# Optimization experiments

Measured on AMD Instinct MI355X. Metric: run time of the kernel, lower is better.

## Reference

```python
import jax, jax.numpy as jnp
import numpy as np

B, V, T, R = 128, 128000, 4096, 64
REP_PENALTY = 1.2   # _rep_penalty (set_repetition_penalty)
MAX_REPS = 3        # _max_reps
REQUIRED_BOOST = 5.0  # _required_boost


def setup_inputs() -> dict:
    key = jax.random.key(0)
    k1, k2, k3, k4 = jax.random.split(key, 4)
    logits = jax.random.normal(k1, (B, V), dtype=jnp.float32)
    generated_so_far = jax.random.randint(k2, (B, T), 0, V, dtype=jnp.int32)
    forbidden_mask = jax.random.bernoulli(k3, 0.01, (V,))
    required_tokens = jax.random.randint(k4, (R,), 0, V, dtype=jnp.int32)
    return {"logits": logits, "generated_so_far": generated_so_far,
            "forbidden_mask": forbidden_mask, "required_tokens": required_tokens}


def reference(logits, generated_so_far, forbidden_mask, required_tokens):
    Bn, Vn = logits.shape
    neg_inf = jnp.float32(-jnp.inf)

    # 1) forbidden tokens -> -inf
    out = jnp.where(forbidden_mask[None, :], neg_inf, logits)

    # per-row token occurrence counts (vectorized bincount) [B, V]
    counts = jnp.zeros((Bn, Vn), jnp.int32).at[
        jnp.arange(Bn)[:, None], generated_so_far
    ].add(1)

    # 2) boost required tokens not yet generated and not forbidden
    present = counts[:, required_tokens] > 0              # [B, R]
    allowed = ~forbidden_mask[required_tokens]            # [R]
    boost = jnp.where((~present) & allowed[None, :],
                      jnp.float32(REQUIRED_BOOST), jnp.float32(0.0))
    out = out.at[:, required_tokens].add(boost)

    # 3) repetition penalty on tokens with count >= MAX_REPS (skip -inf)
    penalized = jnp.where(out > 0, out / REP_PENALTY, out * REP_PENALTY)
    out = jnp.where((counts >= MAX_REPS) & (out != neg_inf), penalized, out)
    return out
```

## Files before the change

### kernel.cpp

```cpp
#include <hip/hip_runtime.h>
#include <cstdint>
#include <cstddef>

#define BB 128
#define VV 128000
#define TT 4096
#define SS 16
#define VR (VV / SS)
#define HW (VR / 4)
#define NT 256

typedef float vf4 __attribute__((ext_vector_type(4)));

__global__ __launch_bounds__(NT) void enforce_kernel(
    const float* __restrict__ logits,
    const int*  __restrict__ gen,
    const unsigned char* __restrict__ maskb,
    const int*  __restrict__ req,
    float* __restrict__ out,
    int R)
{
  __shared__ unsigned hist[HW];
  __shared__ unsigned reqw[HW];
  __shared__ unsigned flz;
  const int tid = threadIdx.x;

  const int L    = blockIdx.x;
  const int xcd  = L & 7;
  const int q    = L >> 3;
  const int s    = q & (SS - 1);
  const int b    = (q >> 4) * 8 + xcd;
  const int vbase = s * VR;

  const int4* grow = (const int4*)(gen + b * TT);
  const int4 g0 = grow[tid];
  const int4 g1 = grow[tid + NT];
  const int4 g2 = grow[tid + 2 * NT];
  const int4 g3 = grow[tid + 3 * NT];
  const int rt = (tid < R) ? req[tid] : -1;

  for (int i = tid; i < HW; i += NT) { hist[i] = 0u; reqw[i] = 0u; }
  if (tid < 64) {
    const uint4* md = (const uint4*)maskb;
    unsigned a = 0u, c = 0u;
#pragma unroll
    for (int k = 0; k < 16; ++k) {
      uint4 w = md[tid + k * 64];
      unsigned o = w.x | w.y | w.z | w.w;
      a |= o & 0x000000FFu;
      c |= o & 0xFFFFFF00u;
    }
    unsigned long long ba = __ballot(a != 0u);
    unsigned long long bc = __ballot(c != 0u);
    if (tid == 0) flz = (ba ? 1u : 0u) | (bc ? 2u : 0u);
  }
  __syncthreads();

  const unsigned agg = flz;
  const int ml = (agg & 2u) ? ((agg & 1u) ? 1 : 2) : ((agg & 1u) ? 0 : 1);

  bool rforb = true;
  if (rt >= 0) {
    if (ml == 1)      rforb = (maskb[rt] != 0);
    else if (ml == 0) rforb = (((const int*)maskb)[rt] != 0);
    else              rforb = (((const float*)maskb)[rt] != 0.0f);
  }

  {
    const int t4[16] = {g0.x, g0.y, g0.z, g0.w, g1.x, g1.y, g1.z, g1.w,
                        g2.x, g2.y, g2.z, g2.w, g3.x, g3.y, g3.z, g3.w};
#pragma unroll
    for (int j = 0; j < 16; ++j) {
      unsigned d = (unsigned)(t4[j] - vbase);
      if (d < (unsigned)VR)
        atomicAdd(&hist[d >> 2], 1u << ((d & 3u) * 8u));
    }
  }

  if (rt >= 0 && !rforb) {
    unsigned d = (unsigned)(rt - vbase);
    if (d < (unsigned)VR)
      atomicAdd(&reqw[d >> 2], 1u << ((d & 3u) * 8u));
  }
  for (int r = tid + NT; r < R; r += NT) {
    int t = req[r];
    unsigned d = (unsigned)(t - vbase);
    if (d < (unsigned)VR) {
      bool fb;
      if (ml == 1)      fb = (maskb[t] != 0);
      else if (ml == 0) fb = (((const int*)maskb)[t] != 0);
      else              fb = (((const float*)maskb)[t] != 0.0f);
      if (!fb) atomicAdd(&reqw[d >> 2], 1u << ((d & 3u) * 8u));
    }
  }
  __syncthreads();

  const vf4* lrow = (const vf4*)(logits + (size_t)b * VV + vbase);
  vf4*       orow = (vf4*)(out + (size_t)b * VV + vbase);
  const unsigned*  m8   = (const unsigned*)(maskb + vbase);
  const int4*      m32  = (const int4*)((const int*)maskb + vbase);
  const float4*    mf32 = (const float4*)((const float*)maskb + vbase);
  const float SENT = __uint_as_float(0xFF7F0000u);
  const float RINV = 1.0f / 1.2f;

  auto load_mask = [&](int i) -> unsigned {
    if (ml == 1) return m8[i];
    if (ml == 0) {
      int4 m = m32[i];
      return (m.x ? 1u : 0u) | (m.y ? 0x100u : 0u) |
             (m.z ? 0x10000u : 0u) | (m.w ? 0x1000000u : 0u);
    }
    float4 m = mf32[i];
    return (m.x != 0.f ? 1u : 0u) | (m.y != 0.f ? 0x100u : 0u) |
           (m.z != 0.f ? 0x10000u : 0u) | (m.w != 0.f ? 0x1000000u : 0u);
  };

  auto compute = [&](vf4 x, unsigned cw, unsigned bw, unsigned fw) -> vf4 {
    vf4 r;
#pragma unroll
    for (int j = 0; j < 4; ++j) {
      float v = x[j];
      unsigned cnt = (cw >> (j * 8)) & 0xFFu;
      float bm = (cnt == 0u) ? (float)((bw >> (j * 8)) & 0xFFu) : 0.0f;
      bool forb = ((fw >> (j * 8)) & 0xFFu) != 0u;
      float fac = (cnt >= 3u) ? ((v > 0.0f) ? RINV : 1.2f) : 1.0f;
      float y = v * fac + 5.0f * bm;
      r[j] = forb ? SENT : y;
    }
    return r;
  };

  for (int i0 = tid; i0 < HW; i0 += 2 * NT) {
    const int i1 = i0 + NT;
    const bool p1 = (i1 < HW);
    vf4 x0 = lrow[i0];
    unsigned f0 = load_mask(i0);
    vf4 x1 = {0.f, 0.f, 0.f, 0.f};
    unsigned f1 = 0u;
    if (p1) { x1 = lrow[i1]; f1 = load_mask(i1); }

    vf4 r0 = compute(x0, hist[i0], reqw[i0], f0);
    orow[i0] = r0;
    if (p1) {
      vf4 r1 = compute(x1, hist[i1], reqw[i1], f1);
      orow[i1] = r1;
    }
  }
}

extern "C" void kernel_launch(void* const* d_in, const int* in_sizes, int n_in,
                              void* d_out, int out_size, void* d_ws, size_t ws_size,
                              hipStream_t stream) {
  const float* logits = (const float*)d_in[0];
  const int*   gen    = (const int*)d_in[1];
  const unsigned char* maskb = (const unsigned char*)d_in[2];
  const int*   req    = (const int*)d_in[3];
  float* out  = (float*)d_out;
  const int R = in_sizes[3];

  enforce_kernel<<<BB * SS, NT, 0, stream>>>(logits, gen, maskb, req, out, R);
}
```

Before: 124.5 us.

## Give each wavefront its own vocab slice and drop block-level barriers

```diff
diff --git a/kernel.cpp b/kernel.cpp
--- a/kernel.cpp
+++ b/kernel.cpp
@@ -5,14 +5,15 @@
 #define BB 128
 #define VV 128000
 #define TT 4096
-#define SS 16
+#define SS 64
 #define VR (VV / SS)
-#define HW (VR / 4)
+#define HWW (VR / 4)
 #define NT 256
+#define NW 4
 
 typedef float vf4 __attribute__((ext_vector_type(4)));
 
-__global__ __launch_bounds__(NT) void enforce_kernel(
+__global__ __launch_bounds__(NT, 8) void enforce_kernel(
     const float* __restrict__ logits,
     const int*  __restrict__ gen,
     const unsigned char* __restrict__ maskb,
@@ -20,69 +21,78 @@
     float* __restrict__ out,
     int R)
 {
-  __shared__ unsigned hist[HW];
-  __shared__ unsigned reqw[HW];
-  __shared__ unsigned flz;
-  const int tid = threadIdx.x;
+  __shared__ unsigned lds[NW * 2 * HWW];
+  const int tid  = threadIdx.x;
+  const int wid  = tid >> 6;
+  const int lane = tid & 63;
 
   const int L    = blockIdx.x;
   const int xcd  = L & 7;
   const int q    = L >> 3;
-  const int s    = q & (SS - 1);
   const int b    = (q >> 4) * 8 + xcd;
+  const int s    = (q & 15) * NW + wid;
   const int vbase = s * VR;
 
+  unsigned* hist = &lds[wid * (2 * HWW)];
+  unsigned* rqw  = hist + HWW;
+
+  const int rt = (lane < R) ? req[lane] : -1;
+
+  for (int i = lane; i < 2 * HWW; i += 64) hist[i] = 0u;
+
   const int4* grow = (const int4*)(gen + b * TT);
-  const int4 g0 = grow[tid];
-  const int4 g1 = grow[tid + NT];
-  const int4 g2 = grow[tid + 2 * NT];
-  const int4 g3 = grow[tid + 3 * NT];
-  const int rt = (tid < R) ? req[tid] : -1;
-
-  for (int i = tid; i < HW; i += NT) { hist[i] = 0u; reqw[i] = 0u; }
-  if (tid < 64) {
-    const uint4* md = (const uint4*)maskb;
-    unsigned a = 0u, c = 0u;
+#pragma unroll 1
+  for (int k = 0; k < 2; ++k) {
+    const int base = k * 8;
+    int4 h0 = grow[lane + (base + 0) * 64];
+    int4 h1 = grow[lane + (base + 1) * 64];
+    int4 h2 = grow[lane + (base + 2) * 64];
+    int4 h3 = grow[lane + (base + 3) * 64];
+    int4 h4 = grow[lane + (base + 4) * 64];
+    int4 h5 = grow[lane + (base + 5) * 64];
+    int4 h6 = grow[lane + (base + 6) * 64];
+    int4 h7 = grow[lane + (base + 7) * 64];
+    const int t32[32] = {h0.x, h0.y, h0.z, h0.w, h1.x, h1.y, h1.z, h1.w,
+                         h2.x, h2.y, h2.z, h2.w, h3.x, h3.y, h3.z, h3.w,
+                         h4.x, h4.y, h4.z, h4.w, h5.x, h5.y, h5.z, h5.w,
+                         h6.x, h6.y, h6.z, h6.w, h7.x, h7.y, h7.z, h7.w};
 #pragma unroll
-    for (int k = 0; k < 16; ++k) {
-      uint4 w = md[tid + k * 64];
-      unsigned o = w.x | w.y | w.z | w.w;
-      a |= o & 0x000000FFu;
-      c |= o & 0xFFFFFF00u;
-    }
-    unsigned long long ba = __ballot(a != 0u);
-    unsigned long long bc = __ballot(c != 0u);
-    if (tid == 0) flz = (ba ? 1u : 0u) | (bc ? 2u : 0u);
-  }
-  __syncthreads();
-
-  const unsigned agg = flz;
-  const int ml = (agg & 2u) ? ((agg & 1u) ? 1 : 2) : ((agg & 1u) ? 0 : 1);
-
-  bool rforb = true;
-  if (rt >= 0) {
-    if (ml == 1)      rforb = (maskb[rt] != 0);
-    else if (ml == 0) rforb = (((const int*)maskb)[rt] != 0);
-    else              rforb = (((const float*)maskb)[rt] != 0.0f);
-  }
-
-  {
-    const int t4[16] = {g0.x, g0.y, g0.z, g0.w, g1.x, g1.y, g1.z, g1.w,
-                        g2.x, g2.y, g2.z, g2.w, g3.x, g3.y, g3.z, g3.w};
-#pragma unroll
-    for (int j = 0; j < 16; ++j) {
-      unsigned d = (unsigned)(t4[j] - vbase);
+    for (int j = 0; j < 32; ++j) {
+      unsigned d = (unsigned)(t32[j] - vbase);
       if (d < (unsigned)VR)
         atomicAdd(&hist[d >> 2], 1u << ((d & 3u) * 8u));
     }
   }
 
-  if (rt >= 0 && !rforb) {
+  unsigned aa = 0u, cc = 0u;
+  {
+    const uint4* md = (const uint4*)maskb;
+#pragma unroll 1
+    for (int k = 0; k < 2; ++k) {
+      const int base = k * 8;
+#pragma unroll
+      for (int t = 0; t < 8; ++t) {
+        uint4 w = md[lane + (base + t) * 64];
+        unsigned o = w.x | w.y | w.z | w.w;
+        aa |= o & 0x000000FFu;
+        cc |= o & 0xFFFFFF00u;
+      }
+    }
+  }
+  const unsigned long long ba = __ballot(aa != 0u);
+  const unsigned long long bc = __ballot(cc != 0u);
+  const int ml = bc ? (ba ? 1 : 2) : (ba ? 0 : 1);
+
+  if (rt >= 0) {
+    bool rforb;
+    if (ml == 1)      rforb = (maskb[rt] != 0);
+    else if (ml == 0) rforb = (((const int*)maskb)[rt] != 0);
+    else              rforb = (((const float*)maskb)[rt] != 0.0f);
     unsigned d = (unsigned)(rt - vbase);
-    if (d < (unsigned)VR)
-      atomicAdd(&reqw[d >> 2], 1u << ((d & 3u) * 8u));
+    if (!rforb && d < (unsigned)VR)
+      atomicAdd(&rqw[d >> 2], 1u << ((d & 3u) * 8u));
   }
-  for (int r = tid + NT; r < R; r += NT) {
+  for (int r = lane + 64; r < R; r += 64) {
     int t = req[r];
     unsigned d = (unsigned)(t - vbase);
     if (d < (unsigned)VR) {
@@ -90,10 +100,9 @@
       if (ml == 1)      fb = (maskb[t] != 0);
       else if (ml == 0) fb = (((const int*)maskb)[t] != 0);
       else              fb = (((const float*)maskb)[t] != 0.0f);
-      if (!fb) atomicAdd(&reqw[d >> 2], 1u << ((d & 3u) * 8u));
+      if (!fb) atomicAdd(&rqw[d >> 2], 1u << ((d & 3u) * 8u));
     }
   }
-  __syncthreads();
 
   const vf4* lrow = (const vf4*)(logits + (size_t)b * VV + vbase);
   vf4*       orow = (vf4*)(out + (size_t)b * VV + vbase);
@@ -130,19 +139,19 @@
     return r;
   };
 
-  for (int i0 = tid; i0 < HW; i0 += 2 * NT) {
-    const int i1 = i0 + NT;
-    const bool p1 = (i1 < HW);
+  for (int i0 = lane; i0 < HWW; i0 += 128) {
+    const int i1 = i0 + 64;
+    const bool p1 = (i1 < HWW);
     vf4 x0 = lrow[i0];
     unsigned f0 = load_mask(i0);
     vf4 x1 = {0.f, 0.f, 0.f, 0.f};
     unsigned f1 = 0u;
     if (p1) { x1 = lrow[i1]; f1 = load_mask(i1); }
 
-    vf4 r0 = compute(x0, hist[i0], reqw[i0], f0);
+    vf4 r0 = compute(x0, hist[i0], rqw[i0], f0);
     orow[i0] = r0;
     if (p1) {
-      vf4 r1 = compute(x1, hist[i1], reqw[i1], f1);
+      vf4 r1 = compute(x1, hist[i1], rqw[i1], f1);
       orow[i1] = r1;
     }
   }
@@ -158,5 +167,5 @@
   float* out  = (float*)d_out;
   const int R = in_sizes[3];
 
-  enforce_kernel<<<BB * SS, NT, 0, stream>>>(logits, gen, maskb, req, out, R);
+  enforce_kernel<<<BB * SS / NW, NT, 0, stream>>>(logits, gen, maskb, req, out, R);
 }
```

New measurement: 139.3 us. 11.9% more time.

## Split into streaming mask kernel plus sparse histogram fixup kernel

Applied to the files above, without the earlier changes.

```diff
diff --git a/kernel.cpp b/kernel.cpp
--- a/kernel.cpp
+++ b/kernel.cpp
@@ -5,145 +5,132 @@
 #define BB 128
 #define VV 128000
 #define TT 4096
-#define SS 16
-#define VR (VV / SS)
-#define HW (VR / 4)
 #define NT 256
+
+#define BSL 4
+#define BVR (VV / BSL)
+#define BHW (BVR / 4)
 
 typedef float vf4 __attribute__((ext_vector_type(4)));
 
-__global__ __launch_bounds__(NT) void enforce_kernel(
+
+__device__ __forceinline__ int block_detect(const unsigned char* maskb,
+                                            unsigned* det, int tid) {
+  if (tid == 0) *det = 0u;
+  __syncthreads();
+  const uint4* md = (const uint4*)maskb;
+  unsigned a = 0u, c = 0u;
+#pragma unroll
+  for (int k = 0; k < 4; ++k) {
+    uint4 w = md[tid + k * NT];
+    unsigned o = w.x | w.y | w.z | w.w;
+    a |= o & 0x000000FFu;
+    c |= o & 0xFFFFFF00u;
+  }
+  unsigned long long ba = __ballot(a != 0u);
+  unsigned long long bc = __ballot(c != 0u);
+  if ((tid & 63) == 0) {
+    unsigned bits = (ba ? 1u : 0u) | (bc ? 2u : 0u);
+    if (bits) atomicOr(det, bits);
+  }
+  __syncthreads();
+  return (*det == 3u) ? 1 : 3;
+}
+
+template<int ML>
+__global__ __launch_bounds__(NT) void stream_kernel(
     const float* __restrict__ logits,
+    const unsigned char* __restrict__ maskb,
+    float* __restrict__ out)
+{
+  int ml = ML;
+  if constexpr (ML == -1) {
+    __shared__ unsigned det;
+    ml = block_detect(maskb, &det, threadIdx.x);
+  }
+  const float SENT = __uint_as_float(0xFF7F0000u);
+  const vf4* lin = (const vf4*)logits;
+  vf4*       o4  = (vf4*)out;
+  const unsigned* m8  = (const unsigned*)maskb;
+  const int4*     m32 = (const int4*)maskb;
+  const unsigned totalw = BB * (VV / 4);
+  const unsigned stride = gridDim.x * NT;
+  for (unsigned i = blockIdx.x * NT + threadIdx.x; i < totalw; i += stride) {
+    const unsigned col = i % (unsigned)(VV / 4);
+    vf4 x = lin[i];
+    unsigned fw;
+    if (ml == 1) {
+      fw = m8[col];
+    } else {
+      int4 m = m32[col];
+      fw = (m.x ? 1u : 0u) | (m.y ? 0x100u : 0u) |
+           (m.z ? 0x10000u : 0u) | (m.w ? 0x1000000u : 0u);
+    }
+    vf4 r;
+#pragma unroll
+    for (int j = 0; j < 4; ++j)
+      r[j] = ((fw >> (j * 8)) & 0xFFu) ? SENT : x[j];
+    o4[i] = r;
+  }
+}
+
+template<int ML>
+__global__ __launch_bounds__(NT) void fixup_kernel(
     const int*  __restrict__ gen,
     const unsigned char* __restrict__ maskb,
     const int*  __restrict__ req,
     float* __restrict__ out,
     int R)
 {
-  __shared__ unsigned hist[HW];
-  __shared__ unsigned reqw[HW];
-  __shared__ unsigned flz;
-  const int tid = threadIdx.x;
+  __shared__ unsigned hist[BHW];
+  int ml = ML;
+  if constexpr (ML == -1) {
+    __shared__ unsigned det;
+    ml = block_detect(maskb, &det, threadIdx.x);
+  }
+  const int tid   = threadIdx.x;
+  const int b     = blockIdx.x >> 2;
+  const int vbase = (blockIdx.x & 3) * BVR;
 
-  const int L    = blockIdx.x;
-  const int xcd  = L & 7;
-  const int q    = L >> 3;
-  const int s    = q & (SS - 1);
-  const int b    = (q >> 4) * 8 + xcd;
-  const int vbase = s * VR;
+  for (int i = tid; i < BHW; i += NT) hist[i] = 0u;
+  __syncthreads();
+
+  const float RINV = 1.0f / 1.2f;
+  auto forb = [&](int t) -> bool {
+    if (ml == 1) return maskb[t] != 0;
+    return ((const int*)maskb)[t] != 0;
+  };
 
   const int4* grow = (const int4*)(gen + b * TT);
-  const int4 g0 = grow[tid];
-  const int4 g1 = grow[tid + NT];
-  const int4 g2 = grow[tid + 2 * NT];
-  const int4 g3 = grow[tid + 3 * NT];
-  const int rt = (tid < R) ? req[tid] : -1;
-
-  for (int i = tid; i < HW; i += NT) { hist[i] = 0u; reqw[i] = 0u; }
-  if (tid < 64) {
-    const uint4* md = (const uint4*)maskb;
-    unsigned a = 0u, c = 0u;
+  for (int i = tid; i < TT / 4; i += NT) {
+    int4 g = grow[i];
+    const int t4[4] = {g.x, g.y, g.z, g.w};
 #pragma unroll
-    for (int k = 0; k < 16; ++k) {
-      uint4 w = md[tid + k * 64];
-      unsigned o = w.x | w.y | w.z | w.w;
-      a |= o & 0x000000FFu;
-      c |= o & 0xFFFFFF00u;
-    }
-    unsigned long long ba = __ballot(a != 0u);
-    unsigned long long bc = __ballot(c != 0u);
-    if (tid == 0) flz = (ba ? 1u : 0u) | (bc ? 2u : 0u);
-  }
-  __syncthreads();
-
-  const unsigned agg = flz;
-  const int ml = (agg & 2u) ? ((agg & 1u) ? 1 : 2) : ((agg & 1u) ? 0 : 1);
-
-  bool rforb = true;
-  if (rt >= 0) {
-    if (ml == 1)      rforb = (maskb[rt] != 0);
-    else if (ml == 0) rforb = (((const int*)maskb)[rt] != 0);
-    else              rforb = (((const float*)maskb)[rt] != 0.0f);
-  }
-
-  {
-    const int t4[16] = {g0.x, g0.y, g0.z, g0.w, g1.x, g1.y, g1.z, g1.w,
-                        g2.x, g2.y, g2.z, g2.w, g3.x, g3.y, g3.z, g3.w};
-#pragma unroll
-    for (int j = 0; j < 16; ++j) {
-      unsigned d = (unsigned)(t4[j] - vbase);
-      if (d < (unsigned)VR)
-        atomicAdd(&hist[d >> 2], 1u << ((d & 3u) * 8u));
-    }
-  }
-
-  if (rt >= 0 && !rforb) {
-    unsigned d = (unsigned)(rt - vbase);
-    if (d < (unsigned)VR)
-      atomicAdd(&reqw[d >> 2], 1u << ((d & 3u) * 8u));
-  }
-  for (int r = tid + NT; r < R; r += NT) {
-    int t = req[r];
-    unsigned d = (unsigned)(t - vbase);
-    if (d < (unsigned)VR) {
-      bool fb;
-      if (ml == 1)      fb = (maskb[t] != 0);
-      else if (ml == 0) fb = (((const int*)maskb)[t] != 0);
-      else              fb = (((const float*)maskb)[t] != 0.0f);
-      if (!fb) atomicAdd(&reqw[d >> 2], 1u << ((d & 3u) * 8u));
+    for (int j = 0; j < 4; ++j) {
+      const int t = t4[j];
+      unsigned d = (unsigned)(t - vbase);
+      if (d < (unsigned)BVR) {
+        const unsigned sh = (d & 3u) * 8u;
+        unsigned old = atomicAdd(&hist[d >> 2], 1u << sh);
+        if (((old >> sh) & 0xFFu) == 2u) {
+          if (!forb(t)) {
+            float* p = out + (size_t)b * VV + t;
+            float v = *p;
+            *p = (v > 0.0f) ? v * RINV : v * 1.2f;
+          }
+        }
+      }
     }
   }
   __syncthreads();
 
-  const vf4* lrow = (const vf4*)(logits + (size_t)b * VV + vbase);
-  vf4*       orow = (vf4*)(out + (size_t)b * VV + vbase);
-  const unsigned*  m8   = (const unsigned*)(maskb + vbase);
-  const int4*      m32  = (const int4*)((const int*)maskb + vbase);
-  const float4*    mf32 = (const float4*)((const float*)maskb + vbase);
-  const float SENT = __uint_as_float(0xFF7F0000u);
-  const float RINV = 1.0f / 1.2f;
-
-  auto load_mask = [&](int i) -> unsigned {
-    if (ml == 1) return m8[i];
-    if (ml == 0) {
-      int4 m = m32[i];
-      return (m.x ? 1u : 0u) | (m.y ? 0x100u : 0u) |
-             (m.z ? 0x10000u : 0u) | (m.w ? 0x1000000u : 0u);
-    }
-    float4 m = mf32[i];
-    return (m.x != 0.f ? 1u : 0u) | (m.y != 0.f ? 0x100u : 0u) |
-           (m.z != 0.f ? 0x10000u : 0u) | (m.w != 0.f ? 0x1000000u : 0u);
-  };
-
-  auto compute = [&](vf4 x, unsigned cw, unsigned bw, unsigned fw) -> vf4 {
-    vf4 r;
-#pragma unroll
-    for (int j = 0; j < 4; ++j) {
-      float v = x[j];
-      unsigned cnt = (cw >> (j * 8)) & 0xFFu;
-      float bm = (cnt == 0u) ? (float)((bw >> (j * 8)) & 0xFFu) : 0.0f;
-      bool forb = ((fw >> (j * 8)) & 0xFFu) != 0u;
-      float fac = (cnt >= 3u) ? ((v > 0.0f) ? RINV : 1.2f) : 1.0f;
-      float y = v * fac + 5.0f * bm;
-      r[j] = forb ? SENT : y;
-    }
-    return r;
-  };
-
-  for (int i0 = tid; i0 < HW; i0 += 2 * NT) {
-    const int i1 = i0 + NT;
-    const bool p1 = (i1 < HW);
-    vf4 x0 = lrow[i0];
-    unsigned f0 = load_mask(i0);
-    vf4 x1 = {0.f, 0.f, 0.f, 0.f};
-    unsigned f1 = 0u;
-    if (p1) { x1 = lrow[i1]; f1 = load_mask(i1); }
-
-    vf4 r0 = compute(x0, hist[i0], reqw[i0], f0);
-    orow[i0] = r0;
-    if (p1) {
-      vf4 r1 = compute(x1, hist[i1], reqw[i1], f1);
-      orow[i1] = r1;
+  for (int r = tid; r < R; r += NT) {
+    int t = req[r];
+    unsigned d = (unsigned)(t - vbase);
+    if (d < (unsigned)BVR) {
+      unsigned cnt = (hist[d >> 2] >> ((d & 3u) * 8u)) & 0xFFu;
+      if (cnt == 0u && !forb(t))
+        atomicAdd(out + (size_t)b * VV + t, 5.0f);
     }
   }
 }
@@ -155,8 +142,28 @@
   const int*   gen    = (const int*)d_in[1];
   const unsigned char* maskb = (const unsigned char*)d_in[2];
   const int*   req    = (const int*)d_in[3];
-  float* out  = (float*)d_out;
-  const int R = in_sizes[3];
+  float* out = (float*)d_out;
 
-  enforce_kernel<<<BB * SS, NT, 0, stream>>>(logits, gen, maskb, req, out, R);
+  int R = in_sizes[3];
+  if (R >= 256 && (R & 3) == 0) R >>= 2;
+
+  int ml;
+  if (in_sizes[0] == BB * VV * 4) {
+    ml = (in_sizes[2] == VV) ? 1 : 3;
+  } else {
+    ml = -1;
+  }
+
+  const int GA = 2048;
+  const int GB = BB * BSL;
+  if (ml == 1) {
+    stream_kernel<1><<<GA, NT, 0, stream>>>(logits, maskb, out);
+    fixup_kernel<1><<<GB, NT, 0, stream>>>(gen, maskb, req, out, R);
+  } else if (ml == 3) {
+    stream_kernel<3><<<GA, NT, 0, stream>>>(logits, maskb, out);
+    fixup_kernel<3><<<GB, NT, 0, stream>>>(gen, maskb, req, out, R);
+  } else {
+    stream_kernel<-1><<<GA, NT, 0, stream>>>(logits, maskb, out);
+    fixup_kernel<-1><<<GB, NT, 0, stream>>>(gen, maskb, req, out, R);
+  }
 }
```

New measurement: 127.0 us. About the same (+2.0%).
